# Optimization experiments

Measured on AMD Instinct MI355X. Metric: run time of the kernel, lower is better.

Reference implementation:

```python
import jax, jax.numpy as jnp
import numpy as np

# TT structure: W is [in_features, out_features] = [4096, 4096]
IN_FACTORS = (16, 16, 16)
OUT_FACTORS = (16, 16, 16)
RANKS = (1, 8, 8, 1)
BATCH = 8192
IN_FEATURES = 4096
OUT_FEATURES = 4096
ITER_NUM = 3
L = 1.0
S = -1.0
EPSILON = 1.0


def tt_dense_matmul(cores, mat):
    """Multiply TT-matrix (cores[k]: [r_{k-1}, m_k, n_k, r_k]) by dense mat [prod(n), P].
    Returns [prod(m), P]. Sequential core contractions, never materializes dense W."""
    P = mat.shape[1]
    data = mat.reshape(1, mat.shape[0], P)  # [r=1, N_rem, T]
    M = 1
    for core in cores:
        r0, m, n, r1 = core.shape
        nrem = data.shape[1]
        d4 = data.reshape(r0, n, nrem // n, -1)            # [r0, n_k, N_rem', T]
        data = jnp.einsum('rmns,rnat->satm', core, d4)      # [r1, N_rem', T, m_k]
        data = data.reshape(r1, nrem // n, -1)              # fold m_k into trailing T
        M *= m
    return data.reshape(P, M).T  # [M, P]


def tt_tt_mul(cores_a, cores_b):
    """TT-matrix product: cores of A [M,K] and B [K,N] -> cores of A@B with Kronecker ranks."""
    out = []
    for ca, cb in zip(cores_a, cores_b):
        a0, m, n, a1 = ca.shape
        b0, n2, l, b1 = cb.shape
        c = jnp.einsum('amnb,cnld->acmlbd', ca, cb)
        out.append(c.reshape(a0 * b0, m, l, a1 * b1))
    return out


def setup_inputs() -> dict:
    key = jax.random.key(0)
    ks = jax.random.split(key, 5)
    x = jax.random.normal(ks[0], (BATCH, IN_FEATURES), dtype=jnp.float32)
    # TT cores of weight W [in, out]: core_k shape [r_{k-1}, in_k, out_k, r_k]
    core_std = 0.3  # glorot-like per-core scale
    cores = []
    for k in range(3):
        shp = (RANKS[k], IN_FACTORS[k], OUT_FACTORS[k], RANKS[k + 1])
        cores.append(core_std * jax.random.normal(ks[k + 1], shp, dtype=jnp.float32))
    bias = 0.01 * jnp.ones((OUT_FEATURES,), dtype=jnp.float32)
    return {"x": x, "core0": cores[0], "core1": cores[1], "core2": cores[2], "bias": bias}


def reference(x, core0, core1, core2, bias):
    cores = [core0, core1, core2]
    # weight_t = t3.transpose(weight): swap in/out mode of each core
    cores_t = [c.transpose(0, 2, 1, 3) for c in cores]  # W^T: [out, in]
    x_t = x.T  # [in, B]
    mv = tt_dense_matmul(cores_t, x_t).T  # x @ W, [B, out]
    # norm-gated shrinkage init
    norm_x = jnp.linalg.norm(x)
    x_l = (mv + bias) / L + jnp.where(norm_x > EPSILON, 0.0, S)
    # G = W^T @ W in TT form (ranks grow to 64)
    G = tt_tt_mul(cores_t, cores)
    for _ in range(1, ITER_NUM):
        nrm = jnp.linalg.norm(x_l)
        term = tt_dense_matmul(G, x_l.T).T  # x_l @ (W^T W), [B, out]
        x_l = x_l - term / L + mv / L + bias + jnp.where(nrm > EPSILON, 0.0, S)
    return x_l
```

## Files before the change

kernel.cpp:

```cpp
#include <hip/hip_runtime.h>
#include <stdint.h>

typedef __bf16 bf16;
typedef __bf16 bf16x4 __attribute__((ext_vector_type(4)));
typedef __bf16 bf16x8 __attribute__((ext_vector_type(8)));
typedef float f32x4 __attribute__((ext_vector_type(4)));

#define GLD_LDS16(g, l)                                                        \
  __builtin_amdgcn_global_load_lds(                                            \
      (const __attribute__((address_space(1))) void*)(g),                      \
      (__attribute__((address_space(3))) void*)(l), 16, 0, 0)

#define BAR() asm volatile("s_barrier" ::: "memory")
#define VMW(n) asm volatile("s_waitcnt vmcnt(" #n ")" ::: "memory")
#define PRIO(x) __builtin_amdgcn_s_setprio(x)

__global__ void k_init(float* s) {
  if (threadIdx.x < 3) s[threadIdx.x] = 0.0f;
}

__global__ void k_cast_ssq(const float* __restrict__ x, bf16* __restrict__ xb,
                           float* __restrict__ ssq, int n4) {
  int tid = blockIdx.x * blockDim.x + threadIdx.x;
  int stride = gridDim.x * blockDim.x;
  const float4* x4 = (const float4*)x;
  bf16x4* xb4 = (bf16x4*)xb;
  float acc = 0.f;
  for (int i = tid; i < n4; i += stride) {
    float4 v = x4[i];
    acc += v.x * v.x + v.y * v.y + v.z * v.z + v.w * v.w;
    bf16x4 b;
    b.x = (bf16)v.x; b.y = (bf16)v.y; b.z = (bf16)v.z; b.w = (bf16)v.w;
    xb4[i] = b;
  }
#pragma unroll
  for (int off = 32; off; off >>= 1) acc += __shfl_down(acc, off);
  __shared__ float red[4];
  if ((threadIdx.x & 63) == 0) red[threadIdx.x >> 6] = acc;
  __syncthreads();
  if (threadIdx.x == 0) atomicAdd(ssq, red[0] + red[1] + red[2] + red[3]);
}

__global__ void k_buildW(const float* __restrict__ c0, const float* __restrict__ c1,
                         const float* __restrict__ c2, bf16* __restrict__ Wt) {
  int t = blockIdx.x * 256 + threadIdx.x;
  int j = t >> 8;
  int i0 = (t >> 4) & 15;
  int i1 = t & 15;
  int j0 = j >> 8, j1 = (j >> 4) & 15, j2 = j & 15;
  float t0[8];
#pragma unroll
  for (int r1 = 0; r1 < 8; ++r1) t0[r1] = c0[(i0 * 16 + j0) * 8 + r1];
  float a[8];
#pragma unroll
  for (int r2 = 0; r2 < 8; ++r2) {
    float s = 0.f;
#pragma unroll
    for (int r1 = 0; r1 < 8; ++r1) s += t0[r1] * c1[((r1 * 16 + i1) * 16 + j1) * 8 + r2];
    a[r2] = s;
  }
  union { bf16 h[16]; bf16x8 v[2]; } u;
#pragma unroll
  for (int i2 = 0; i2 < 16; ++i2) {
    float s = 0.f;
#pragma unroll
    for (int r2 = 0; r2 < 8; ++r2) s += a[r2] * c2[(r2 * 16 + i2) * 16 + j2];
    u.h[i2] = (bf16)s;
  }
  bf16* dst = Wt + (size_t)j * 4096 + i0 * 256 + i1 * 16;
  ((bf16x8*)dst)[0] = u.v[0];
  ((bf16x8*)dst)[1] = u.v[1];
}

__global__ __launch_bounds__(256) void k_gcores(const float* __restrict__ c0,
                                                const float* __restrict__ c1,
                                                const float* __restrict__ c2,
                                                float* __restrict__ g0,
                                                float* __restrict__ g1,
                                                float* __restrict__ g2) {
  int tid = blockIdx.x * 256 + threadIdx.x;
  if (tid < 16384) {
    int jj = tid >> 6, p1 = tid & 63;
    int j0 = jj >> 4, j0p = jj & 15, r1 = p1 >> 3, r1p = p1 & 7;
    float s = 0.f;
#pragma unroll
    for (int i0 = 0; i0 < 16; ++i0)
      s += c0[(i0 * 16 + j0) * 8 + r1] * c0[(i0 * 16 + j0p) * 8 + r1p];
    g0[tid] = s;
  } else if (tid < 32768) {
    int k = tid - 16384;
    int p2 = k >> 8, jj = k & 255;
    int r2 = p2 >> 3, r2p = p2 & 7, j2 = jj >> 4, j2p = jj & 15;
    float s = 0.f;
#pragma unroll
    for (int i2 = 0; i2 < 16; ++i2)
      s += c2[(r2 * 16 + i2) * 16 + j2] * c2[(r2p * 16 + i2) * 16 + j2p];
    g2[k] = s;
  } else {
    int k = tid - 32768;
    int p2 = k & 63, rest = k >> 6;
    int j1p = rest & 15, j1 = (rest >> 4) & 15, p1 = rest >> 8;
    int r1 = p1 >> 3, r1p = p1 & 7, r2 = p2 >> 3, r2p = p2 & 7;
    float s = 0.f;
#pragma unroll
    for (int i1 = 0; i1 < 16; ++i1)
      s += c1[((r1 * 16 + i1) * 16 + j1) * 8 + r2] *
           c1[((r1p * 16 + i1) * 16 + j1p) * 8 + r2p];
    g1[k] = s;
  }
}

__global__ __launch_bounds__(256) void k_buildG(const float* __restrict__ g0,
                                                const float* __restrict__ g1,
                                                const float* __restrict__ g2,
                                                bf16* __restrict__ G) {
  __shared__ float s_g2[16384];
  __shared__ float s_g1[4096];
  __shared__ float s_g0t[16384];
  const int t = threadIdx.x;
  const int j1 = blockIdx.x >> 4, j1p = blockIdx.x & 15;
  const int jj1 = j1 * 16 + j1p;

  const float4* g2f4 = (const float4*)g2;
  float4* sg2f4 = (float4*)s_g2;
  for (int k = t; k < 4096; k += 256) sg2f4[k] = g2f4[k];
  const float4* g1f4 = (const float4*)g1;
  float4* sg1f4 = (float4*)s_g1;
  for (int k = t; k < 1024; k += 256) {
    int p1 = k >> 4, q = k & 15;
    sg1f4[k] = g1f4[(p1 * 256 + jj1) * 16 + q];
  }
#pragma unroll
  for (int q = 0; q < 16; ++q) {
    float4 v = ((const float4*)g0)[t * 16 + q];
    s_g0t[(q * 4 + 0) * 256 + t] = v.x;
    s_g0t[(q * 4 + 1) * 256 + t] = v.y;
    s_g0t[(q * 4 + 2) * 256 + t] = v.z;
    s_g0t[(q * 4 + 3) * 256 + t] = v.w;
  }
  __syncthreads();

  float m[64];
#pragma unroll
  for (int i = 0; i < 64; ++i) m[i] = 0.f;
#pragma unroll 4
  for (int p1 = 0; p1 < 64; ++p1) {
    float av = s_g0t[p1 * 256 + t];
#pragma unroll
    for (int q = 0; q < 16; ++q) {
      float4 v = ((const float4*)s_g1)[p1 * 16 + q];
      m[q * 4 + 0] += av * v.x; m[q * 4 + 1] += av * v.y;
      m[q * 4 + 2] += av * v.z; m[q * 4 + 3] += av * v.w;
    }
  }

  const int j0 = t >> 4, j0p = t & 15;
  bf16* gb = G + (size_t)(j0 * 256 + j1 * 16) * 4096 + (j0p * 256 + j1p * 16);
  for (int j2 = 0; j2 < 16; ++j2) {
    float o[16];
#pragma unroll
    for (int i = 0; i < 16; ++i) o[i] = 0.f;
#pragma unroll
    for (int p2 = 0; p2 < 64; ++p2) {
      const float4* r = (const float4*)s_g2 + p2 * 64 + j2 * 4;
#pragma unroll
      for (int q = 0; q < 4; ++q) {
        float4 v = r[q];
        o[q * 4 + 0] += m[p2] * v.x; o[q * 4 + 1] += m[p2] * v.y;
        o[q * 4 + 2] += m[p2] * v.z; o[q * 4 + 3] += m[p2] * v.w;
      }
    }
    union { bf16 h[16]; bf16x8 v[2]; } u;
#pragma unroll
    for (int i = 0; i < 16; ++i) u.h[i] = (bf16)o[i];
    bf16* d = gb + (size_t)j2 * 4096;
    ((bf16x8*)d)[0] = u.v[0];
    ((bf16x8*)d)[1] = u.v[1];
  }
}

#define STAGE_A(h, kt, b)                                                              \
  do {                                                                                 \
    GLD_LDS16(srcA + (size_t)((h) * 128) * K + (kt) * 64,                              \
              smem + (b) * 65536 + (h) * 16384 + wofs);                                \
    GLD_LDS16(srcA + (size_t)((h) * 128 + 64) * K + (kt) * 64,                         \
              smem + (b) * 65536 + (h) * 16384 + 8192 + wofs);                         \
  } while (0)
#define STAGE_B(h, kt, b)                                                              \
  do {                                                                                 \
    GLD_LDS16(srcB + (size_t)((h) * 128) * K + (kt) * 64,                              \
              smem + (b) * 65536 + 32768 + (h) * 16384 + wofs);                        \
    GLD_LDS16(srcB + (size_t)((h) * 128 + 64) * K + (kt) * 64,                         \
              smem + (b) * 65536 + 32768 + (h) * 16384 + 8192 + wofs);                 \
  } while (0)
#define LDA(ms, b)                                                                     \
  do {                                                                                 \
    const char* s_ = smem + (b) * 65536 + (ms) * 16384 + aRow;                         \
    _Pragma("unroll") for (int mi_ = 0; mi_ < 4; ++mi_) {                              \
      af[mi_][0] = *(const bf16x8*)(s_ + mi_ * 2048 + cb0);                            \
      af[mi_][1] = *(const bf16x8*)(s_ + mi_ * 2048 + cb1);                            \
    }                                                                                  \
  } while (0)
#define LDBX(ns, b, DST)                                                               \
  do {                                                                                 \
    const char* s_ = smem + (b) * 65536 + 32768 + (ns) * 16384 + bRow;                 \
    _Pragma("unroll") for (int ni_ = 0; ni_ < 2; ++ni_) {                              \
      DST[ni_][0] = *(const bf16x8*)(s_ + ni_ * 2048 + cb0);                           \
      DST[ni_][1] = *(const bf16x8*)(s_ + ni_ * 2048 + cb1);                           \
    }                                                                                  \
  } while (0)
#define MQ(ms, ns, BSRC)                                                               \
  do {                                                                                 \
    PRIO(1);                                                                           \
    _Pragma("unroll") for (int mi_ = 0; mi_ < 4; ++mi_)                                \
    _Pragma("unroll") for (int ni_ = 0; ni_ < 2; ++ni_)                                \
    _Pragma("unroll") for (int ks_ = 0; ks_ < 2; ++ks_)                                \
        acc[(ms) * 4 + mi_][(ns) * 2 + ni_] =                                          \
            __builtin_amdgcn_mfma_f32_16x16x32_bf16(                                   \
                af[mi_][ks_], BSRC[ni_][ks_],                                          \
                acc[(ms) * 4 + mi_][(ns) * 2 + ni_], 0, 0, 0);                         \
    PRIO(0);                                                                           \
  } while (0)

__device__ __forceinline__ void run_core(const bf16* __restrict__ Ag,
                                         const bf16* __restrict__ Bg, const int K,
                                         const int bx, const int by, char* smem,
                                         f32x4 (&acc)[8][4]) {
  const int t = threadIdx.x;
  const int w = t >> 6, lane = t & 63;
  const int q = lane >> 4, lr = lane & 15;
  const int wm = w & 1, wn = w >> 1;

  const int r0 = t >> 3;
  const int ksrc = (t & 7) ^ (r0 & 7);
  const bf16* srcA = Ag + (size_t)(by * 256 + r0) * K + ksrc * 8;
  const bf16* srcB = Bg + (size_t)(bx * 256 + r0) * K + ksrc * 8;
  const int wofs = w << 10;

  const int aRow = (wm * 64 + lr) * 128;
  const int bRow = (wn * 32 + lr) * 128;
  const int cb0 = ((q ^ (lr & 7)) << 4);
  const int cb1 = (((4 + q) ^ (lr & 7)) << 4);

#pragma unroll
  for (int i = 0; i < 8; ++i)
#pragma unroll
    for (int j = 0; j < 4; ++j) acc[i][j] = (f32x4){0.f, 0.f, 0.f, 0.f};

  bf16x8 af[4][2];
  bf16x8 bfr1[2][2];
  bf16x8 bfr0A[2][2];
  bf16x8 bfr0B[2][2];

  STAGE_A(0, 0, 0); STAGE_B(0, 0, 0); STAGE_B(1, 0, 0); STAGE_A(1, 0, 0);
  STAGE_A(0, 1, 1); STAGE_B(0, 1, 1); STAGE_B(1, 1, 1);
  VMW(6);
  BAR();
  LDBX(0, 0, bfr0A);

  const int NT = K >> 6;
#pragma unroll 1
  for (int tt = 0; tt < (NT >> 1) - 1; ++tt) {
    const int T = tt << 1;
    STAGE_A(1, T + 1, 1);
    LDA(0, 0);
    MQ(0, 0, bfr0A);
    BAR();
    STAGE_A(0, T + 2, 0);
    LDBX(1, 0, bfr1);
    MQ(0, 1, bfr1);
    BAR();
    STAGE_B(0, T + 2, 0);
    LDA(1, 0);
    MQ(1, 1, bfr1);
    VMW(4);
    BAR();
    STAGE_B(1, T + 2, 0);
    LDBX(0, 1, bfr0B);
    MQ(1, 0, bfr0A);
    BAR();
    STAGE_A(1, T + 2, 0);
    LDA(0, 1);
    MQ(0, 0, bfr0B);
    BAR();
    STAGE_A(0, T + 3, 1);
    LDBX(1, 1, bfr1);
    MQ(0, 1, bfr1);
    BAR();
    STAGE_B(0, T + 3, 1);
    LDA(1, 1);
    MQ(1, 1, bfr1);
    VMW(4);
    BAR();
    STAGE_B(1, T + 3, 1);
    LDBX(0, 0, bfr0A);
    MQ(1, 0, bfr0B);
    BAR();
  }

  STAGE_A(1, NT - 1, 1);
  LDA(0, 0);
  MQ(0, 0, bfr0A); BAR();
  LDBX(1, 0, bfr1);
  MQ(0, 1, bfr1); BAR();
  LDA(1, 0);
  MQ(1, 1, bfr1);
  VMW(0);
  BAR();
  LDBX(0, 1, bfr0B);
  MQ(1, 0, bfr0A);
  BAR();
  LDA(0, 1);
  MQ(0, 0, bfr0B); BAR();
  LDBX(1, 1, bfr1);
  MQ(0, 1, bfr1); BAR();
  LDA(1, 1);
  MQ(1, 1, bfr1); BAR();
  MQ(1, 0, bfr0B);
}

template <int MODE>
__global__ __launch_bounds__(512, 2) void k_gemm(
    const bf16* __restrict__ A, const bf16* __restrict__ Bt, int M, int N, int K,
    const float* __restrict__ bias, const bf16* __restrict__ xl0,
    const bf16* __restrict__ xl_prev, float* f32_out, bf16* __restrict__ bf_out,
    const float* __restrict__ ssq_a, const float* __restrict__ ssq_b,
    float* __restrict__ ssq_out) {
  const int nb = gridDim.x * gridDim.y;
  const int lin = blockIdx.y * gridDim.x + blockIdx.x;
  const int sw = (lin & 7) * (nb >> 3) + (lin >> 3);
  const int bx = sw % gridDim.x, by = sw / gridDim.x;
  __shared__ char smem[131072];

  float gate = 0.f;
  if constexpr (MODE == 0) {
    gate = (*ssq_a > 1.0f) ? 0.f : -1.f;
  } else {
    float g0v = (*ssq_a > 1.0f) ? 0.f : -1.f;
    float gtv = (*ssq_b > 1.0f) ? 0.f : -1.f;
    gate = gtv - g0v;
  }
  VMW(0);

  f32x4 acc[8][4];
  run_core(A, Bt, K, bx, by, smem, acc);

  const int t = threadIdx.x;
  const int w = t >> 6, lane = t & 63;
  const int q = lane >> 4, lr = lane & 15;
  const int wm = w & 1, wn = w >> 1;
  float ssql = 0.f;
#pragma unroll
  for (int mi = 0; mi < 8; ++mi) {
    const int grow = by * 256 + ((mi & 4) ? 128 : 0) + wm * 64 + (mi & 3) * 16 + q * 4;
#pragma unroll
    for (int r = 0; r < 4; ++r) {
      const size_t rowb = (size_t)(grow + r) * N;
#pragma unroll
      for (int ni = 0; ni < 4; ++ni) {
        const int gcol = bx * 256 + ((ni & 2) ? 128 : 0) + wn * 32 + (ni & 1) * 16 + lr;
        const size_t idx = rowb + gcol;
        float v = acc[mi][ni][r];
        if constexpr (MODE == 0) {
          float xl = v + bias[gcol] + gate;
          bf_out[idx] = (bf16)xl;
          ssql += xl * xl;
        } else if constexpr (MODE == 2) {
          float xl = 2.0f * (float)xl0[idx] - v + gate;
          bf_out[idx] = (bf16)xl;
          ssql += xl * xl;
        } else {
          f32_out[idx] = (float)xl_prev[idx] - v + (float)xl0[idx] + gate;
        }
      }
    }
  }
  if constexpr (MODE == 0 || MODE == 2) {
#pragma unroll
    for (int off = 32; off; off >>= 1) ssql += __shfl_down(ssql, off);
    __syncthreads();
    float* red = (float*)smem;
    if (lane == 0) red[w] = ssql;
    __syncthreads();
    if (t == 0) {
      float s = 0.f;
#pragma unroll
      for (int i = 0; i < 8; ++i) s += red[i];
      atomicAdd(ssq_out, s);
    }
  }
}

extern "C" void kernel_launch(void* const* d_in, const int* in_sizes, int n_in,
                              void* d_out, int out_size, void* d_ws, size_t ws_size,
                              hipStream_t stream) {
  const float* x = (const float*)d_in[0];
  const float* c0 = (const float*)d_in[1];
  const float* c1 = (const float*)d_in[2];
  const float* c2 = (const float*)d_in[3];
  const float* bias = (const float*)d_in[4];
  float* out = (float*)d_out;

  const int B = 8192, F = 4096;
  char* ws = (char*)d_ws;
  float* scal = (float*)ws;
  bf16* xbf = (bf16*)(ws + 256);
  bf16* Wt = (bf16*)(ws + 256 + (size_t)67108864);
  bf16* G = (bf16*)(ws + 256 + (size_t)100663296);
  bf16* xl0 = (bf16*)(ws + 256 + (size_t)134217728);
  bf16* xl1 = xbf;
  float* g0 = (float*)xl0;
  float* g2 = g0 + 16384;
  float* g1 = g2 + 16384;

  k_init<<<1, 64, 0, stream>>>(scal);
  k_cast_ssq<<<1024, 256, 0, stream>>>(x, xbf, &scal[0], B * F / 4);
  k_buildW<<<4096, 256, 0, stream>>>(c0, c1, c2, Wt);

  k_gcores<<<4224, 256, 0, stream>>>(c0, c1, c2, g0, g1, g2);
  k_buildG<<<256, 256, 0, stream>>>(g0, g1, g2, G);

  dim3 g1d(F / 256, B / 256);
  k_gemm<0><<<g1d, 512, 0, stream>>>(xbf, Wt, B, F, F, bias, nullptr, nullptr,
                                     nullptr, xl0, &scal[0], nullptr, &scal[1]);
  k_gemm<2><<<g1d, 512, 0, stream>>>(xl0, G, B, F, F, nullptr, xl0, nullptr,
                                     nullptr, xl1, &scal[0], &scal[1], &scal[2]);
  k_gemm<3><<<g1d, 512, 0, stream>>>(xl1, G, B, F, F, nullptr, xl0, xl1,
                                     out, nullptr, &scal[0], &scal[2], nullptr);
}
```

Before: 983.0 us.

## Restructure GEMM main loop, register-tile buildG, vectorize buildW, fold init

The GEMM K-loop goes from an eight-phase schedule with staggered B-fragment registers to a four-phase schedule. Each phase now loads both B fragments and issues two MFMA quads per barrier, which halves the barrier count but changes how loads overlap with compute. The buildG second stage becomes an 8x16 register-tiled outer product: the intermediate m values are staged through shared memory, so each g2 load is reused across eight rows. buildW gets vectorized float4 loads of the core, and the scalar zeroing moves into buildW so the separate init launch is gone.

```diff
diff --git a/kernel.cpp b/kernel.cpp
--- a/kernel.cpp
+++ b/kernel.cpp
@@ -14,10 +14,6 @@
 #define BAR() asm volatile("s_barrier" ::: "memory")
 #define VMW(n) asm volatile("s_waitcnt vmcnt(" #n ")" ::: "memory")
 #define PRIO(x) __builtin_amdgcn_s_setprio(x)
-
-__global__ void k_init(float* s) {
-  if (threadIdx.x < 3) s[threadIdx.x] = 0.0f;
-}
 
 __global__ void k_cast_ssq(const float* __restrict__ x, bf16* __restrict__ xb,
                            float* __restrict__ ssq, int n4) {
@@ -41,23 +37,35 @@
   if (threadIdx.x == 0) atomicAdd(ssq, red[0] + red[1] + red[2] + red[3]);
 }
 
-__global__ void k_buildW(const float* __restrict__ c0, const float* __restrict__ c1,
-                         const float* __restrict__ c2, bf16* __restrict__ Wt) {
-  int t = blockIdx.x * 256 + threadIdx.x;
-  int j = t >> 8;
-  int i0 = (t >> 4) & 15;
-  int i1 = t & 15;
-  int j0 = j >> 8, j1 = (j >> 4) & 15, j2 = j & 15;
+__global__ __launch_bounds__(256) void k_buildW(const float* __restrict__ c0,
+                                                const float* __restrict__ c1,
+                                                const float* __restrict__ c2,
+                                                bf16* __restrict__ Wt,
+                                                float* __restrict__ scal) {
+  if (blockIdx.x == 0 && threadIdx.x < 3) scal[threadIdx.x] = 0.0f;
+  const int j = blockIdx.x;
+  const int j0 = j >> 8, j1 = (j >> 4) & 15, j2 = j & 15;
+  const int t = threadIdx.x;
+  const int i0 = t >> 4, i1 = t & 15;
   float t0[8];
-#pragma unroll
-  for (int r1 = 0; r1 < 8; ++r1) t0[r1] = c0[(i0 * 16 + j0) * 8 + r1];
+  {
+    float4 v0 = *(const float4*)&c0[(i0 * 16 + j0) * 8];
+    float4 v1 = *(const float4*)&c0[(i0 * 16 + j0) * 8 + 4];
+    t0[0] = v0.x; t0[1] = v0.y; t0[2] = v0.z; t0[3] = v0.w;
+    t0[4] = v1.x; t0[5] = v1.y; t0[6] = v1.z; t0[7] = v1.w;
+  }
   float a[8];
 #pragma unroll
-  for (int r2 = 0; r2 < 8; ++r2) {
-    float s = 0.f;
-#pragma unroll
-    for (int r1 = 0; r1 < 8; ++r1) s += t0[r1] * c1[((r1 * 16 + i1) * 16 + j1) * 8 + r2];
-    a[r2] = s;
+  for (int r2 = 0; r2 < 8; ++r2) a[r2] = 0.f;
+#pragma unroll
+  for (int r1 = 0; r1 < 8; ++r1) {
+    const float* row = &c1[((r1 * 16 + i1) * 16 + j1) * 8];
+    float4 u0 = *(const float4*)row;
+    float4 u1 = *(const float4*)(row + 4);
+    a[0] += t0[r1] * u0.x; a[1] += t0[r1] * u0.y;
+    a[2] += t0[r1] * u0.z; a[3] += t0[r1] * u0.w;
+    a[4] += t0[r1] * u1.x; a[5] += t0[r1] * u1.y;
+    a[6] += t0[r1] * u1.z; a[7] += t0[r1] * u1.w;
   }
   union { bf16 h[16]; bf16x8 v[2]; } u;
 #pragma unroll
@@ -116,7 +124,7 @@
                                                 bf16* __restrict__ G) {
   __shared__ float s_g2[16384];
   __shared__ float s_g1[4096];
-  __shared__ float s_g0t[16384];
+  __shared__ float s_g0m[16384];
   const int t = threadIdx.x;
   const int j1 = blockIdx.x >> 4, j1p = blockIdx.x & 15;
   const int jj1 = j1 * 16 + j1p;
@@ -133,10 +141,10 @@
 #pragma unroll
   for (int q = 0; q < 16; ++q) {
     float4 v = ((const float4*)g0)[t * 16 + q];
-    s_g0t[(q * 4 + 0) * 256 + t] = v.x;
-    s_g0t[(q * 4 + 1) * 256 + t] = v.y;
-    s_g0t[(q * 4 + 2) * 256 + t] = v.z;
-    s_g0t[(q * 4 + 3) * 256 + t] = v.w;
+    s_g0m[(q * 4 + 0) * 256 + t] = v.x;
+    s_g0m[(q * 4 + 1) * 256 + t] = v.y;
+    s_g0m[(q * 4 + 2) * 256 + t] = v.z;
+    s_g0m[(q * 4 + 3) * 256 + t] = v.w;
   }
   __syncthreads();
 
@@ -145,7 +153,7 @@
   for (int i = 0; i < 64; ++i) m[i] = 0.f;
 #pragma unroll 4
   for (int p1 = 0; p1 < 64; ++p1) {
-    float av = s_g0t[p1 * 256 + t];
+    float av = s_g0m[p1 * 256 + t];
 #pragma unroll
     for (int q = 0; q < 16; ++q) {
       float4 v = ((const float4*)s_g1)[p1 * 16 + q];
@@ -153,29 +161,49 @@
       m[q * 4 + 2] += av * v.z; m[q * 4 + 3] += av * v.w;
     }
   }
-
-  const int j0 = t >> 4, j0p = t & 15;
-  bf16* gb = G + (size_t)(j0 * 256 + j1 * 16) * 4096 + (j0p * 256 + j1p * 16);
-  for (int j2 = 0; j2 < 16; ++j2) {
-    float o[16];
-#pragma unroll
-    for (int i = 0; i < 16; ++i) o[i] = 0.f;
-#pragma unroll
+  __syncthreads();
+#pragma unroll
+  for (int p2 = 0; p2 < 64; ++p2) s_g0m[p2 * 256 + t] = m[p2];
+  __syncthreads();
+
+  const int bcol = (t & 15) * 16;
+  const int j2 = t & 15;
+#pragma unroll 1
+  for (int rep = 0; rep < 2; ++rep) {
+    const int r0 = (((t >> 4) + rep * 16)) * 8;
+    float acc2[8][16];
+#pragma unroll
+    for (int i = 0; i < 8; ++i)
+#pragma unroll
+      for (int c = 0; c < 16; ++c) acc2[i][c] = 0.f;
+#pragma unroll 2
     for (int p2 = 0; p2 < 64; ++p2) {
-      const float4* r = (const float4*)s_g2 + p2 * 64 + j2 * 4;
+      float4 mv0 = *(const float4*)&s_g0m[p2 * 256 + r0];
+      float4 mv1 = *(const float4*)&s_g0m[p2 * 256 + r0 + 4];
+      float mv[8] = {mv0.x, mv0.y, mv0.z, mv0.w, mv1.x, mv1.y, mv1.z, mv1.w};
+      float gv[16];
 #pragma unroll
       for (int q = 0; q < 4; ++q) {
-        float4 v = r[q];
-        o[q * 4 + 0] += m[p2] * v.x; o[q * 4 + 1] += m[p2] * v.y;
-        o[q * 4 + 2] += m[p2] * v.z; o[q * 4 + 3] += m[p2] * v.w;
+        float4 v = *(const float4*)&s_g2[p2 * 256 + bcol + q * 4];
+        gv[q * 4 + 0] = v.x; gv[q * 4 + 1] = v.y;
+        gv[q * 4 + 2] = v.z; gv[q * 4 + 3] = v.w;
       }
+#pragma unroll
+      for (int i = 0; i < 8; ++i)
+#pragma unroll
+        for (int c = 0; c < 16; ++c) acc2[i][c] += mv[i] * gv[c];
     }
-    union { bf16 h[16]; bf16x8 v[2]; } u;
-#pragma unroll
-    for (int i = 0; i < 16; ++i) u.h[i] = (bf16)o[i];
-    bf16* d = gb + (size_t)j2 * 4096;
-    ((bf16x8*)d)[0] = u.v[0];
-    ((bf16x8*)d)[1] = u.v[1];
+#pragma unroll
+    for (int i = 0; i < 8; ++i) {
+      const int jj0 = r0 + i;
+      const int j0 = jj0 >> 4, j0p = jj0 & 15;
+      bf16* d = G + (size_t)(j0 * 256 + j1 * 16 + j2) * 4096 + (j0p * 256 + j1p * 16);
+      union { bf16 h[16]; bf16x8 v[2]; } u;
+#pragma unroll
+      for (int c = 0; c < 16; ++c) u.h[c] = (bf16)acc2[i][c];
+      ((bf16x8*)d)[0] = u.v[0];
+      ((bf16x8*)d)[1] = u.v[1];
+    }
   }
 }
 
@@ -201,15 +229,15 @@
       af[mi_][1] = *(const bf16x8*)(s_ + mi_ * 2048 + cb1);                            \
     }                                                                                  \
   } while (0)
-#define LDBX(ns, b, DST)                                                               \
+#define LDB(ns, b)                                                                     \
   do {                                                                                 \
     const char* s_ = smem + (b) * 65536 + 32768 + (ns) * 16384 + bRow;                 \
     _Pragma("unroll") for (int ni_ = 0; ni_ < 2; ++ni_) {                              \
-      DST[ni_][0] = *(const bf16x8*)(s_ + ni_ * 2048 + cb0);                           \
-      DST[ni_][1] = *(const bf16x8*)(s_ + ni_ * 2048 + cb1);                           \
+      bfr[ns][ni_][0] = *(const bf16x8*)(s_ + ni_ * 2048 + cb0);                       \
+      bfr[ns][ni_][1] = *(const bf16x8*)(s_ + ni_ * 2048 + cb1);                       \
     }                                                                                  \
   } while (0)
-#define MQ(ms, ns, BSRC)                                                               \
+#define MQ(ms, ns)                                                                     \
   do {                                                                                 \
     PRIO(1);                                                                           \
     _Pragma("unroll") for (int mi_ = 0; mi_ < 4; ++mi_)                                \
@@ -217,7 +245,7 @@
     _Pragma("unroll") for (int ks_ = 0; ks_ < 2; ++ks_)                                \
         acc[(ms) * 4 + mi_][(ns) * 2 + ni_] =                                          \
             __builtin_amdgcn_mfma_f32_16x16x32_bf16(                                   \
-                af[mi_][ks_], BSRC[ni_][ks_],                                          \
+                af[mi_][ks_], bfr[ns][ni_][ks_],                                       \
                 acc[(ms) * 4 + mi_][(ns) * 2 + ni_], 0, 0, 0);                         \
     PRIO(0);                                                                           \
   } while (0)
@@ -248,75 +276,49 @@
     for (int j = 0; j < 4; ++j) acc[i][j] = (f32x4){0.f, 0.f, 0.f, 0.f};
 
   bf16x8 af[4][2];
-  bf16x8 bfr1[2][2];
-  bf16x8 bfr0A[2][2];
-  bf16x8 bfr0B[2][2];
+  bf16x8 bfr[2][2][2];
 
   STAGE_A(0, 0, 0); STAGE_B(0, 0, 0); STAGE_B(1, 0, 0); STAGE_A(1, 0, 0);
   STAGE_A(0, 1, 1); STAGE_B(0, 1, 1); STAGE_B(1, 1, 1);
   VMW(6);
   BAR();
-  LDBX(0, 0, bfr0A);
 
   const int NT = K >> 6;
 #pragma unroll 1
-  for (int tt = 0; tt < (NT >> 1) - 1; ++tt) {
-    const int T = tt << 1;
-    STAGE_A(1, T + 1, 1);
-    LDA(0, 0);
-    MQ(0, 0, bfr0A);
+  for (int tt = 0; tt + 3 < NT; tt += 2) {
+    STAGE_A(1, tt + 1, 1);
+    LDB(0, 0); LDA(0, 0); LDB(1, 0);
+    MQ(0, 0); MQ(0, 1);
     BAR();
-    STAGE_A(0, T + 2, 0);
-    LDBX(1, 0, bfr1);
-    MQ(0, 1, bfr1);
+    STAGE_A(0, tt + 2, 0); STAGE_B(0, tt + 2, 0); STAGE_B(1, tt + 2, 0);
+    LDA(1, 0);
+    MQ(1, 1); MQ(1, 0);
+    VMW(6);
     BAR();
-    STAGE_B(0, T + 2, 0);
-    LDA(1, 0);
-    MQ(1, 1, bfr1);
-    VMW(4);
+    STAGE_A(1, tt + 2, 0);
+    LDB(0, 1); LDA(0, 1); LDB(1, 1);
+    MQ(0, 0); MQ(0, 1);
     BAR();
-    STAGE_B(1, T + 2, 0);
-    LDBX(0, 1, bfr0B);
-    MQ(1, 0, bfr0A);
+    STAGE_A(0, tt + 3, 1); STAGE_B(0, tt + 3, 1); STAGE_B(1, tt + 3, 1);
+    LDA(1, 1);
+    MQ(1, 1); MQ(1, 0);
+    VMW(6);
     BAR();
-    STAGE_A(1, T + 2, 0);
-    LDA(0, 1);
-    MQ(0, 0, bfr0B);
-    BAR();
-    STAGE_A(0, T + 3, 1);
-    LDBX(1, 1, bfr1);
-    MQ(0, 1, bfr1);
-    BAR();
-    STAGE_B(0, T + 3, 1);
-    LDA(1, 1);
-    MQ(1, 1, bfr1);
-    VMW(4);
-    BAR();
-    STAGE_B(1, T + 3, 1);
-    LDBX(0, 0, bfr0A);
-    MQ(1, 0, bfr0B);
-    BAR();
   }
 
   STAGE_A(1, NT - 1, 1);
-  LDA(0, 0);
-  MQ(0, 0, bfr0A); BAR();
-  LDBX(1, 0, bfr1);
-  MQ(0, 1, bfr1); BAR();
+  LDB(0, 0); LDA(0, 0); LDB(1, 0);
+  MQ(0, 0); MQ(0, 1);
+  BAR();
   LDA(1, 0);
-  MQ(1, 1, bfr1);
+  MQ(1, 1); MQ(1, 0);
   VMW(0);
   BAR();
-  LDBX(0, 1, bfr0B);
-  MQ(1, 0, bfr0A);
+  LDB(0, 1); LDA(0, 1); LDB(1, 1);
+  MQ(0, 0); MQ(0, 1);
   BAR();
-  LDA(0, 1);
-  MQ(0, 0, bfr0B); BAR();
-  LDBX(1, 1, bfr1);
-  MQ(0, 1, bfr1); BAR();
   LDA(1, 1);
-  MQ(1, 1, bfr1); BAR();
-  MQ(1, 0, bfr0B);
+  MQ(1, 1); MQ(1, 0);
 }
 
 template <int MODE>
@@ -413,9 +415,8 @@
   float* g2 = g0 + 16384;
   float* g1 = g2 + 16384;
 
-  k_init<<<1, 64, 0, stream>>>(scal);
+  k_buildW<<<4096, 256, 0, stream>>>(c0, c1, c2, Wt, scal);
   k_cast_ssq<<<1024, 256, 0, stream>>>(x, xbf, &scal[0], B * F / 4);
-  k_buildW<<<4096, 256, 0, stream>>>(c0, c1, c2, Wt);
 
   k_gcores<<<4224, 256, 0, stream>>>(c0, c1, c2, g0, g1, g2);
   k_buildG<<<256, 256, 0, stream>>>(g0, g1, g2, G);
```

After: 985.1 us. Within noise of the previous version (+0.2%).
